# Optimization experiments

Measured on AMD Instinct MI355X. Metric: run time of the kernel, lower is better.

Reference implementation:

```python
import jax, jax.numpy as jnp
import numpy as np

EPS = 1e-5

def _rmsnorm(x, w):
    # Faithful to the repo's rms_norm: divides by sqrt(SUM of squares + eps)
    # (the .mean(-1) in the original acts on a size-1 dim and is a no-op).
    rms = jnp.sqrt(jnp.sum(x * x, axis=-1, keepdims=True) + EPS)
    return (x / rms) * w

def _conv2d(x, w, b):
    # x: (N, C=m, H=L, W=2*d_model), w: (O, I, 3, 3), padding=1 -> SAME
    y = jax.lax.conv_general_dilated(
        x, w, window_strides=(1, 1), padding='SAME',
        dimension_numbers=('NCHW', 'OIHW', 'NCHW'))
    return y + b[None, :, None, None]

def _ssm(x, fc1_W, fc1_b, fc2_W, fc2_b, A):
    # x: (b, m, l, d) with d = 2*d_model; state dim n = 128
    Bm = x @ fc2_W.T + fc2_b                       # (b,m,l,n); C = fc2(x) as well -> identical
    delta = jax.nn.softplus(x @ fc1_W.T + fc1_b)   # (b,m,l,d)
    dA = jnp.exp(jnp.einsum('bmld,dn->bmldn', delta, A))   # (b,m,l,d,n)
    dB = jnp.einsum('bmld,bmln->bmldn', delta, Bm)         # (b,m,l,d,n)
    h_new = dA + x[..., None] * dB                 # h is initialized to ones and never updated
    return jnp.einsum('bmln,bmldn->bmld', Bm, h_new)

def setup_inputs() -> dict:
    key = jax.random.key(0)
    ks = jax.random.split(key, 16)
    B, M, L, D = 1, 2, 256, 256
    D2, S = 2 * D, 128
    def rn(k, shape, scale=0.02):
        return jax.random.normal(k, shape, jnp.float32) * scale
    return {
        'x': jax.random.normal(ks[0], (B, M, L, D), jnp.float32),
        'mouth': jax.random.normal(ks[1], (B, M, L, D), jnp.float32),
        'norm_w': jnp.ones((D,), jnp.float32),
        'inp_W': rn(ks[2], (D2, D)), 'inp_b': rn(ks[3], (D2,)),
        'out_W': rn(ks[4], (D, D2)), 'out_b': jnp.ones((D,), jnp.float32),  # bias init 1.0
        'Dlin_W': rn(ks[5], (D2, D)), 'Dlin_b': rn(ks[6], (D2,)),
        'conv_W': rn(ks[7], (M, M, 3, 3), 0.1), 'conv_b': rn(ks[8], (M,)),
        'fc1_W': rn(ks[9], (D2, D2)), 'fc1_b': rn(ks[10], (D2,)),
        'fc2_W': rn(ks[11], (S, D2)), 'fc2_b': rn(ks[12], (S,)),
        'A': rn(ks[13], (D2, S), 0.05),
    }

def reference(x, mouth, norm_w, inp_W, inp_b, out_W, out_b, Dlin_W, Dlin_b,
              conv_W, conv_b, fc1_W, fc1_b, fc2_W, fc2_b, A):
    x_n = _rmsnorm(x, norm_w)
    m_n = _rmsnorm(mouth, norm_w)
    x_p = x_n @ inp_W.T + inp_b        # (B,M,L,2D)
    m_p = m_n @ inp_W.T + inp_b
    x_c = jax.nn.silu(_conv2d(x_p, conv_W, conv_b))
    m_c = jax.nn.silu(_conv2d(m_p, conv_W, conv_b))
    x_s = jax.nn.silu(_ssm(x_c, fc1_W, fc1_b, fc2_W, fc2_b, A))
    m_s = jax.nn.silu(_ssm(m_c, fc1_W, fc1_b, fc2_W, fc2_b, A))
    res = jax.nn.silu(x_n @ Dlin_W.T + Dlin_b)   # D(x) uses the normed x
    comb = x_s * res + m_s * res
    return comb @ out_W.T + out_b
```

## Files before the change

### kernel.cpp

```cpp
#include <hip/hip_runtime.h>
#include <hip/hip_bf16.h>
#include <math.h>


#define D_   256
#define D2_  512
#define S_   128

typedef short  bf16x8 __attribute__((ext_vector_type(8)));
typedef short  bf16x4 __attribute__((ext_vector_type(4)));
typedef float  f32x4  __attribute__((ext_vector_type(4)));

__device__ __forceinline__ float silu_f(float v) {
    return v / (1.f + __expf(-v));
}
__device__ __forceinline__ float softplus_f(float v) {
    return fmaxf(v, 0.f) + log1pf(__expf(-fabsf(v)));
}
__device__ __forceinline__ short f2bf(float f) {
    __hip_bfloat16 h = __float2bfloat16(f);
    return reinterpret_cast<short&>(h);
}

template<bool NORM, int ACT1, int ACT2>
__global__ __launch_bounds__(256) void gemm_mfma_k(
        const float* __restrict__ A0, const float* __restrict__ A1,
        const float* __restrict__ nw,
        const float* __restrict__ W1, const float* __restrict__ bias1,
        float* __restrict__ O1, int nct1, int ldo1, int n1,
        const float* __restrict__ W2, const float* __restrict__ bias2,
        float* __restrict__ O2, int nct2, int ldo2, int K) {
    __shared__ __align__(16) short a_lds[2][32 * 56];
    __shared__ __align__(16) short w_lds[2][64 * 56];
    const int b = blockIdx.x;
    const float *W, *bias; float* O; int ldo, act, rt, ct;
    if (b < n1) { W = W1; bias = bias1; O = O1; ldo = ldo1; act = ACT1; rt = b / nct1; ct = b % nct1; }
    else { int bb = b - n1; W = W2; bias = bias2; O = O2; ldo = ldo2; act = ACT2; rt = bb / nct2; ct = bb % nct2; }
    const int r0 = rt * 32, c0 = ct * 64;
    const int t = threadIdx.x;
    const int sr = t >> 3, sk = (t & 7) << 2;
    const int wc = t >> 2, wk = (t & 3) << 3;
    const int rowA = r0 + sr;
    const float* rowbase = (rowA < 512) ? (A0 + (size_t)rowA * K)
                                        : (A1 + (size_t)(rowA - 512) * K);
    float ascale = 1.f;
    if (NORM) {
        float ssum = 0.f;
        const float* rp = rowbase + (t & 7) * 32;
#pragma unroll
        for (int q = 0; q < 8; ++q) {
            float4 v = *(const float4*)(rp + q * 4);
            ssum += v.x * v.x + v.y * v.y + v.z * v.z + v.w * v.w;
        }
        ssum += __shfl_xor(ssum, 1);
        ssum += __shfl_xor(ssum, 2);
        ssum += __shfl_xor(ssum, 4);
        ascale = 1.f / sqrtf(ssum + 1e-5f);
    }
    const float* Ag = rowbase + sk;
    const float* Wg = W + (size_t)(c0 + wc) * K + wk;
    float4 areg  = *(const float4*)Ag;
    float4 wrega = *(const float4*)Wg;
    float4 wregb = *(const float4*)(Wg + 4);
    float4 nwreg = NORM ? *(const float4*)(nw + sk) : make_float4(0.f, 0.f, 0.f, 0.f);
    const int wv = t >> 6, lane = t & 63;
    const int aoff  = ((wv & 1) * 16 + (lane & 15)) * 56 + (lane >> 4) * 8;
    const int boff0 = ((wv >> 1) * 32 + (lane & 15)) * 56 + (lane >> 4) * 8;
    const int boff1 = boff0 + 16 * 56;
    f32x4 acc0 = {0.f, 0.f, 0.f, 0.f};
    f32x4 acc1 = {0.f, 0.f, 0.f, 0.f};
    const int nch = K >> 5;
    for (int ch = 0; ch < nch; ++ch) {
        const int p = ch & 1;
        float4 a = areg;
        if (NORM) {
            a.x *= ascale * nwreg.x; a.y *= ascale * nwreg.y;
            a.z *= ascale * nwreg.z; a.w *= ascale * nwreg.w;
        }
        bf16x4 av; av[0] = f2bf(a.x); av[1] = f2bf(a.y); av[2] = f2bf(a.z); av[3] = f2bf(a.w);
        *(bf16x4*)&a_lds[p][sr * 56 + sk] = av;
        bf16x8 wv8;
        wv8[0] = f2bf(wrega.x); wv8[1] = f2bf(wrega.y); wv8[2] = f2bf(wrega.z); wv8[3] = f2bf(wrega.w);
        wv8[4] = f2bf(wregb.x); wv8[5] = f2bf(wregb.y); wv8[6] = f2bf(wregb.z); wv8[7] = f2bf(wregb.w);
        *(bf16x8*)&w_lds[p][wc * 56 + wk] = wv8;
        __syncthreads();
        if (ch + 1 < nch) {
            const int ko = (ch + 1) << 5;
            areg  = *(const float4*)(Ag + ko);
            wrega = *(const float4*)(Wg + ko);
            wregb = *(const float4*)(Wg + ko + 4);
            if (NORM) nwreg = *(const float4*)(nw + ko + sk);
        }
        bf16x8 af  = *(const bf16x8*)&a_lds[p][aoff];
        bf16x8 bf0 = *(const bf16x8*)&w_lds[p][boff0];
        bf16x8 bf1 = *(const bf16x8*)&w_lds[p][boff1];
        acc0 = __builtin_amdgcn_mfma_f32_16x16x32_bf16(af, bf0, acc0, 0, 0, 0);
        acc1 = __builtin_amdgcn_mfma_f32_16x16x32_bf16(af, bf1, acc1, 0, 0, 0);
    }
    const int rowE = r0 + (wv & 1) * 16 + (lane >> 4) * 4;
    const int colE = c0 + (wv >> 1) * 32 + (lane & 15);
#pragma unroll
    for (int cb = 0; cb < 2; ++cb) {
        const f32x4 acc = cb ? acc1 : acc0;
        const int col = colE + cb * 16;
        const float bv = bias[col];
#pragma unroll
        for (int i = 0; i < 4; ++i) {
            float v = acc[i] + bv;
            if (act == 1)      v = silu_f(v);
            else if (act == 2) v = softplus_f(v);
            O[(size_t)(rowE + i) * ldo + col] = v;
        }
    }
}

__global__ __launch_bounds__(256) void conv_silu_k(
        const float* __restrict__ xp, const float* __restrict__ cW,
        const float* __restrict__ cb, float* __restrict__ xc) {
    const int idx = blockIdx.x * 256 + threadIdx.x;
    const int w0 = (idx & 127) * 4;
    const int l  = (idx >> 7) & 255;
    const int o  = (idx >> 15) & 1;
    const int tt = idx >> 16;
    const float cbv = cb[o];
    float a[4] = {cbv, cbv, cbv, cbv};
#pragma unroll
    for (int ii = 0; ii < 2; ++ii) {
        const float* base = xp + (size_t)((tt * 2 + ii) * 256) * 512;
#pragma unroll
        for (int dh = -1; dh <= 1; ++dh) {
            const int ll = l + dh;
            if (ll < 0 || ll > 255) continue;
            const float* p = base + (size_t)ll * 512 + w0;
            float4 mid = *(const float4*)p;
            float vm1 = (w0 > 0)   ? p[-1] : 0.f;
            float vp4 = (w0 < 508) ? p[4]  : 0.f;
            const float v[6] = {vm1, mid.x, mid.y, mid.z, mid.w, vp4};
            const float* cwp = &cW[((o * 2 + ii) * 3 + (dh + 1)) * 3];
#pragma unroll
            for (int j = 0; j < 4; ++j)
                a[j] += v[j] * cwp[0] + v[j + 1] * cwp[1] + v[j + 2] * cwp[2];
        }
    }
    float4 r = make_float4(silu_f(a[0]), silu_f(a[1]), silu_f(a[2]), silu_f(a[3]));
    *(float4*)(xc + (size_t)idx * 4) = r;
}

__global__ __launch_bounds__(512) void ssm_out_k(
        const float* __restrict__ xc, const float* __restrict__ delta,
        const float* __restrict__ Bm, const float* __restrict__ A,
        const float* __restrict__ res, const float* __restrict__ outW,
        const float* __restrict__ outb, float* __restrict__ out) {
    __shared__ float Bms[2][2][S_];
    __shared__ float combs[2][D2_];
    __shared__ float red[8];
    const int tid = threadIdx.x;
    const int m  = blockIdx.x >> 7;
    const int l0 = (blockIdx.x & 127) << 1;

    {
        const int g = tid >> 7;
        const int tt = g >> 1, lr = g & 1, n = tid & 127;
        const int rg = tt * 512 + m * 256 + l0 + lr;
        float bv = Bm[(size_t)rg * S_ + n];
        Bms[tt][lr][n] = bv;
        float sq = bv * bv;
        for (int off = 32; off; off >>= 1) sq += __shfl_xor(sq, off);
        if ((tid & 63) == 0) red[tid >> 6] = sq;
    }
    __syncthreads();
    {
        const int d = tid;
        float s2[2][2];
#pragma unroll
        for (int g = 0; g < 4; ++g) s2[g >> 1][g & 1] = red[2 * g] + red[2 * g + 1];
        float dl[2][2], xcv[2][2], rsv[2];
#pragma unroll
        for (int tt = 0; tt < 2; ++tt)
#pragma unroll
            for (int lr = 0; lr < 2; ++lr) {
                const size_t r = (size_t)(tt * 512 + m * 256 + l0 + lr);
                dl[tt][lr]  = delta[r * D2_ + d];
                xcv[tt][lr] = xc[r * D2_ + d];
            }
        rsv[0] = res[(size_t)(m * 256 + l0) * D2_ + d];
        rsv[1] = res[(size_t)(m * 256 + l0 + 1) * D2_ + d];
        float accs[2][2] = {};
        const float4* arow = (const float4*)(A + (size_t)d * S_);
        for (int k4 = 0; k4 < 32; ++k4) {
            float4 a4 = arow[k4];
            const int n = k4 * 4;
#pragma unroll
            for (int cmp = 0; cmp < 4; ++cmp) {
                float a = (cmp == 0) ? a4.x : (cmp == 1) ? a4.y : (cmp == 2) ? a4.z : a4.w;
#pragma unroll
                for (int tt = 0; tt < 2; ++tt)
#pragma unroll
                    for (int lr = 0; lr < 2; ++lr)
                        accs[tt][lr] += Bms[tt][lr][n + cmp] * __expf(dl[tt][lr] * a);
            }
        }
#pragma unroll
        for (int lr = 0; lr < 2; ++lr) {
            float sx = accs[0][lr] + xcv[0][lr] * dl[0][lr] * s2[0][lr];
            float sm = accs[1][lr] + xcv[1][lr] * dl[1][lr] * s2[1][lr];
            combs[lr][d] = (silu_f(sx) + silu_f(sm)) * rsv[lr];
        }
    }
    __syncthreads();
    {
        const int wv = tid >> 6, lane = tid & 63;
        const int j = lane & 15, cg = lane >> 4;
#pragma unroll
        for (int rnd = 0; rnd < 8; ++rnd) {
            const int c = wv * 32 + rnd * 4 + cg;
            const float4* wrow = (const float4*)(outW + (size_t)c * D2_);
            float a0 = 0.f, a1 = 0.f;
#pragma unroll
            for (int it = 0; it < 8; ++it) {
                const int k = it * 64 + j * 4;
                float4 w4 = wrow[it * 16 + j];
                a0 += w4.x * combs[0][k] + w4.y * combs[0][k + 1]
                    + w4.z * combs[0][k + 2] + w4.w * combs[0][k + 3];
                a1 += w4.x * combs[1][k] + w4.y * combs[1][k + 1]
                    + w4.z * combs[1][k + 2] + w4.w * combs[1][k + 3];
            }
            a0 += __shfl_xor(a0, 1); a0 += __shfl_xor(a0, 2);
            a0 += __shfl_xor(a0, 4); a0 += __shfl_xor(a0, 8);
            a1 += __shfl_xor(a1, 1); a1 += __shfl_xor(a1, 2);
            a1 += __shfl_xor(a1, 4); a1 += __shfl_xor(a1, 8);
            if (j == 0) {
                const float b = outb[c];
                out[(size_t)(m * 256 + l0)     * D_ + c] = a0 + b;
                out[(size_t)(m * 256 + l0 + 1) * D_ + c] = a1 + b;
            }
        }
    }
}

extern "C" void kernel_launch(void* const* d_in, const int* in_sizes, int n_in,
                              void* d_out, int out_size, void* d_ws, size_t ws_size,
                              hipStream_t stream) {
    const float* x      = (const float*)d_in[0];
    const float* mouth  = (const float*)d_in[1];
    const float* norm_w = (const float*)d_in[2];
    const float* inp_W  = (const float*)d_in[3];
    const float* inp_b  = (const float*)d_in[4];
    const float* out_W  = (const float*)d_in[5];
    const float* out_b  = (const float*)d_in[6];
    const float* Dlin_W = (const float*)d_in[7];
    const float* Dlin_b = (const float*)d_in[8];
    const float* conv_W = (const float*)d_in[9];
    const float* conv_b = (const float*)d_in[10];
    const float* fc1_W  = (const float*)d_in[11];
    const float* fc1_b  = (const float*)d_in[12];
    const float* fc2_W  = (const float*)d_in[13];
    const float* fc2_b  = (const float*)d_in[14];
    const float* A      = (const float*)d_in[15];

    float* ws    = (float*)d_ws;
    float* xp    = ws;
    float* xc    = xp + 1024 * 512;
    float* res   = xc + 1024 * 512;
    float* Bmb   = res + 512 * 512;
    float* delta = xp;
    float* out   = (float*)d_out;

    gemm_mfma_k<true, 0, 1><<<384, 256, 0, stream>>>(
        x, mouth, norm_w,
        inp_W, inp_b, xp, 8, 512, 256,
        Dlin_W, Dlin_b, res, 8, 512, 256);
    conv_silu_k<<<512, 256, 0, stream>>>(xp, conv_W, conv_b, xc);
    gemm_mfma_k<false, 2, 0><<<320, 256, 0, stream>>>(
        xc, xc + (size_t)512 * 512, nullptr,
        fc1_W, fc1_b, delta, 8, 512, 256,
        fc2_W, fc2_b, Bmb, 2, 128, 512);
    ssm_out_k<<<256, 512, 0, stream>>>(xc, delta, Bmb, A, res,
                                       out_W, out_b, out);
}
```

Before: 136.1 us.

## Fuse conv, fc1/fc2 projections and SSM output into one kernel

Replaces the separate conv+silu kernel, the MFMA GEMM for fc1/fc2 and the SSM/output kernel with a single kernel. Each block stages the halo rows of xp in shared memory, computes the conv, then does the fc1/fc2 matvecs in fp32 CUDA-core FMAs with shuffle reductions, and feeds the results to the existing SSM stage. This removes two launches and the global round-trips of xc, delta and Bm. In exchange, each of the 256 blocks rereads the full fc1/fc2 weights from L2 and gives up MFMA for those GEMMs, which may make the fused kernel compute-bound.

```diff
diff --git a/kernel.cpp b/kernel.cpp
--- a/kernel.cpp
+++ b/kernel.cpp
@@ -114,43 +114,16 @@
     }
 }
 
-__global__ __launch_bounds__(256) void conv_silu_k(
-        const float* __restrict__ xp, const float* __restrict__ cW,
-        const float* __restrict__ cb, float* __restrict__ xc) {
-    const int idx = blockIdx.x * 256 + threadIdx.x;
-    const int w0 = (idx & 127) * 4;
-    const int l  = (idx >> 7) & 255;
-    const int o  = (idx >> 15) & 1;
-    const int tt = idx >> 16;
-    const float cbv = cb[o];
-    float a[4] = {cbv, cbv, cbv, cbv};
-#pragma unroll
-    for (int ii = 0; ii < 2; ++ii) {
-        const float* base = xp + (size_t)((tt * 2 + ii) * 256) * 512;
-#pragma unroll
-        for (int dh = -1; dh <= 1; ++dh) {
-            const int ll = l + dh;
-            if (ll < 0 || ll > 255) continue;
-            const float* p = base + (size_t)ll * 512 + w0;
-            float4 mid = *(const float4*)p;
-            float vm1 = (w0 > 0)   ? p[-1] : 0.f;
-            float vp4 = (w0 < 508) ? p[4]  : 0.f;
-            const float v[6] = {vm1, mid.x, mid.y, mid.z, mid.w, vp4};
-            const float* cwp = &cW[((o * 2 + ii) * 3 + (dh + 1)) * 3];
-#pragma unroll
-            for (int j = 0; j < 4; ++j)
-                a[j] += v[j] * cwp[0] + v[j + 1] * cwp[1] + v[j + 2] * cwp[2];
-        }
-    }
-    float4 r = make_float4(silu_f(a[0]), silu_f(a[1]), silu_f(a[2]), silu_f(a[3]));
-    *(float4*)(xc + (size_t)idx * 4) = r;
-}
-
-__global__ __launch_bounds__(512) void ssm_out_k(
-        const float* __restrict__ xc, const float* __restrict__ delta,
-        const float* __restrict__ Bm, const float* __restrict__ A,
-        const float* __restrict__ res, const float* __restrict__ outW,
+__global__ __launch_bounds__(512) void mega2_k(
+        const float* __restrict__ xp,   const float* __restrict__ res,
+        const float* __restrict__ convW, const float* __restrict__ convB,
+        const float* __restrict__ fc1W, const float* __restrict__ fc1b,
+        const float* __restrict__ fc2W, const float* __restrict__ fc2b,
+        const float* __restrict__ A,    const float* __restrict__ outW,
         const float* __restrict__ outb, float* __restrict__ out) {
+    __shared__ float xph[2][2][4][512];
+    __shared__ float xcs[2][2][512];
+    __shared__ float deltas[2][2][512];
     __shared__ float Bms[2][2][S_];
     __shared__ float combs[2][D2_];
     __shared__ float red[8];
@@ -158,12 +131,123 @@
     const int m  = blockIdx.x >> 7;
     const int l0 = (blockIdx.x & 127) << 1;
 
-    {
-        const int g = tid >> 7;
-        const int tt = g >> 1, lr = g & 1, n = tid & 127;
-        const int rg = tt * 512 + m * 256 + l0 + lr;
-        float bv = Bm[(size_t)rg * S_ + n];
-        Bms[tt][lr][n] = bv;
+#pragma unroll
+    for (int jj = 0; jj < 4; ++jj) {
+        int f   = tid + jj * 512;
+        int w4  = f & 127;
+        int row = f >> 7;
+        int tt = row >> 3, ii = (row >> 2) & 1, h = row & 3;
+        int l = l0 - 1 + h;
+        float4 v = make_float4(0.f, 0.f, 0.f, 0.f);
+        if (l >= 0 && l <= 255)
+            v = *(const float4*)(xp + (size_t)(tt * 512 + ii * 256 + l) * 512 + w4 * 4);
+        *(float4*)&xph[tt][ii][h][w4 * 4] = v;
+    }
+    __syncthreads();
+    {
+        const int w = tid;
+        float cw[2][3][3];
+#pragma unroll
+        for (int ii = 0; ii < 2; ++ii)
+#pragma unroll
+            for (int dh = 0; dh < 3; ++dh)
+#pragma unroll
+                for (int dw = 0; dw < 3; ++dw)
+                    cw[ii][dh][dw] = convW[((m * 2 + ii) * 3 + dh) * 3 + dw];
+        const float cb = convB[m];
+#pragma unroll
+        for (int tt = 0; tt < 2; ++tt)
+#pragma unroll
+            for (int lr = 0; lr < 2; ++lr) {
+                float acc = cb;
+#pragma unroll
+                for (int ii = 0; ii < 2; ++ii)
+#pragma unroll
+                    for (int dh = 0; dh < 3; ++dh) {
+                        const float* src = &xph[tt][ii][lr + dh][0];
+                        if (w >= 1)   acc += src[w - 1] * cw[ii][dh][0];
+                                      acc += src[w    ] * cw[ii][dh][1];
+                        if (w <= 510) acc += src[w + 1] * cw[ii][dh][2];
+                    }
+                xcs[tt][lr][w] = silu_f(acc);
+            }
+    }
+    __syncthreads();
+    {
+        const int g = tid >> 4;
+        const int j = tid & 15;
+#pragma unroll 2
+        for (int rnd = 0; rnd < 16; ++rnd) {
+            const int c = rnd * 32 + g;
+            const float4* wrow = (const float4*)(fc1W + (size_t)c * 512);
+            float a00 = 0.f, a01 = 0.f, a10 = 0.f, a11 = 0.f;
+#pragma unroll
+            for (int it = 0; it < 8; ++it) {
+                const int k = it * 64 + j * 4;
+                float4 w4 = wrow[it * 16 + j];
+                a00 += w4.x * xcs[0][0][k] + w4.y * xcs[0][0][k + 1]
+                     + w4.z * xcs[0][0][k + 2] + w4.w * xcs[0][0][k + 3];
+                a01 += w4.x * xcs[0][1][k] + w4.y * xcs[0][1][k + 1]
+                     + w4.z * xcs[0][1][k + 2] + w4.w * xcs[0][1][k + 3];
+                a10 += w4.x * xcs[1][0][k] + w4.y * xcs[1][0][k + 1]
+                     + w4.z * xcs[1][0][k + 2] + w4.w * xcs[1][0][k + 3];
+                a11 += w4.x * xcs[1][1][k] + w4.y * xcs[1][1][k + 1]
+                     + w4.z * xcs[1][1][k + 2] + w4.w * xcs[1][1][k + 3];
+            }
+#pragma unroll
+            for (int off = 1; off < 16; off <<= 1) {
+                a00 += __shfl_xor(a00, off);
+                a01 += __shfl_xor(a01, off);
+                a10 += __shfl_xor(a10, off);
+                a11 += __shfl_xor(a11, off);
+            }
+            if (j == 0) {
+                const float b = fc1b[c];
+                deltas[0][0][c] = softplus_f(a00 + b);
+                deltas[0][1][c] = softplus_f(a01 + b);
+                deltas[1][0][c] = softplus_f(a10 + b);
+                deltas[1][1][c] = softplus_f(a11 + b);
+            }
+        }
+#pragma unroll
+        for (int rnd = 0; rnd < 4; ++rnd) {
+            const int c = rnd * 32 + g;
+            const float4* wrow = (const float4*)(fc2W + (size_t)c * 512);
+            float a00 = 0.f, a01 = 0.f, a10 = 0.f, a11 = 0.f;
+#pragma unroll
+            for (int it = 0; it < 8; ++it) {
+                const int k = it * 64 + j * 4;
+                float4 w4 = wrow[it * 16 + j];
+                a00 += w4.x * xcs[0][0][k] + w4.y * xcs[0][0][k + 1]
+                     + w4.z * xcs[0][0][k + 2] + w4.w * xcs[0][0][k + 3];
+                a01 += w4.x * xcs[0][1][k] + w4.y * xcs[0][1][k + 1]
+                     + w4.z * xcs[0][1][k + 2] + w4.w * xcs[0][1][k + 3];
+                a10 += w4.x * xcs[1][0][k] + w4.y * xcs[1][0][k + 1]
+                     + w4.z * xcs[1][0][k + 2] + w4.w * xcs[1][0][k + 3];
+                a11 += w4.x * xcs[1][1][k] + w4.y * xcs[1][1][k + 1]
+                     + w4.z * xcs[1][1][k + 2] + w4.w * xcs[1][1][k + 3];
+            }
+#pragma unroll
+            for (int off = 1; off < 16; off <<= 1) {
+                a00 += __shfl_xor(a00, off);
+                a01 += __shfl_xor(a01, off);
+                a10 += __shfl_xor(a10, off);
+                a11 += __shfl_xor(a11, off);
+            }
+            if (j == 0) {
+                const float b = fc2b[c];
+                Bms[0][0][c] = a00 + b;
+                Bms[0][1][c] = a01 + b;
+                Bms[1][0][c] = a10 + b;
+                Bms[1][1][c] = a11 + b;
+            }
+        }
+    }
+    __syncthreads();
+    {
+        const int g4 = tid >> 7;
+        const int tt = g4 >> 1, lr = g4 & 1, n = tid & 127;
+        float bv = Bms[tt][lr][n];
         float sq = bv * bv;
         for (int off = 32; off; off >>= 1) sq += __shfl_xor(sq, off);
         if ((tid & 63) == 0) red[tid >> 6] = sq;
@@ -173,15 +257,14 @@
         const int d = tid;
         float s2[2][2];
 #pragma unroll
-        for (int g = 0; g < 4; ++g) s2[g >> 1][g & 1] = red[2 * g] + red[2 * g + 1];
+        for (int g4 = 0; g4 < 4; ++g4) s2[g4 >> 1][g4 & 1] = red[2 * g4] + red[2 * g4 + 1];
         float dl[2][2], xcv[2][2], rsv[2];
 #pragma unroll
         for (int tt = 0; tt < 2; ++tt)
 #pragma unroll
             for (int lr = 0; lr < 2; ++lr) {
-                const size_t r = (size_t)(tt * 512 + m * 256 + l0 + lr);
-                dl[tt][lr]  = delta[r * D2_ + d];
-                xcv[tt][lr] = xc[r * D2_ + d];
+                dl[tt][lr]  = deltas[tt][lr][d];
+                xcv[tt][lr] = xcs[tt][lr][d];
             }
         rsv[0] = res[(size_t)(m * 256 + l0) * D2_ + d];
         rsv[1] = res[(size_t)(m * 256 + l0 + 1) * D2_ + d];
@@ -258,23 +341,16 @@
     const float* fc2_b  = (const float*)d_in[14];
     const float* A      = (const float*)d_in[15];
 
-    float* ws    = (float*)d_ws;
-    float* xp    = ws;
-    float* xc    = xp + 1024 * 512;
-    float* res   = xc + 1024 * 512;
-    float* Bmb   = res + 512 * 512;
-    float* delta = xp;
-    float* out   = (float*)d_out;
+    float* ws  = (float*)d_ws;
+    float* xp  = ws;
+    float* res = xp + 1024 * 512;
+    float* out = (float*)d_out;
 
     gemm_mfma_k<true, 0, 1><<<384, 256, 0, stream>>>(
         x, mouth, norm_w,
         inp_W, inp_b, xp, 8, 512, 256,
         Dlin_W, Dlin_b, res, 8, 512, 256);
-    conv_silu_k<<<512, 256, 0, stream>>>(xp, conv_W, conv_b, xc);
-    gemm_mfma_k<false, 2, 0><<<320, 256, 0, stream>>>(
-        xc, xc + (size_t)512 * 512, nullptr,
-        fc1_W, fc1_b, delta, 8, 512, 256,
-        fc2_W, fc2_b, Bmb, 2, 128, 512);
-    ssm_out_k<<<256, 512, 0, stream>>>(xc, delta, Bmb, A, res,
-                                       out_W, out_b, out);
-}
+    mega2_k<<<256, 512, 0, stream>>>(xp, res, conv_W, conv_b,
+                                     fc1_W, fc1_b, fc2_W, fc2_b,
+                                     A, out_W, out_b, out);
+}
```

Measured after the change: 157.8 us. 16.0% more time.
